# Kernel optimization log

Hardware: AMD Instinct MI355X
Metric: run time of the kernel (lower is better)

Reference implementation:

```python
import jax, jax.numpy as jnp
import numpy as np

SL, BS, HS = 2048, 2, 1024
FFN, E, TOP_K = 4096, 8, 2


def setup_inputs() -> dict:
    key = jax.random.key(0)
    k1, k2, k3, k4, k5 = jax.random.split(key, 5)
    x = jax.random.normal(k1, (SL, BS, HS), dtype=jnp.float32)
    expert_weights = jax.random.uniform(k2, (SL * BS, TOP_K), dtype=jnp.float32)
    expert_indices = jax.random.randint(k3, (SL * BS, TOP_K), 0, E, dtype=jnp.int32)
    w1 = jax.random.normal(k4, (E, HS, FFN), dtype=jnp.float32) * 0.02
    w2 = jax.random.normal(k5, (E, FFN, HS), dtype=jnp.float32) * 0.02
    return {"x": x, "expert_weights": expert_weights,
            "expert_indices": expert_indices, "w1": w1, "w2": w2}


def reference(x, expert_weights, expert_indices, w1, w2):
    # Dropless MoE: y[t] = sum_k expert_weights[t,k] * MLP_{expert_indices[t,k]}(x[t])
    # Equivalent to megablocks sort/gather/grouped-GEMM/scatter pipeline, expressed
    # as a fixed loop over the (small) expert axis with masked weighted combine.
    sl, bs, hs = x.shape
    xf = x.reshape(-1, hs)                       # [T, hs]
    ew = expert_weights.reshape(xf.shape[0], -1)  # [T, k]
    ei = expert_indices.reshape(xf.shape[0], -1)  # [T, k]
    out = jnp.zeros_like(xf)
    for e in range(w1.shape[0]):
        h = jnp.dot(jax.nn.gelu(jnp.dot(xf, w1[e])), w2[e])   # [T, hs]
        coef = jnp.sum(jnp.where(ei == e, ew, 0.0), axis=-1)  # [T]
        out = out + coef[:, None] * h
    return out.reshape(sl, bs, hs)
```

## Files before the change

### kernel.cpp

```cpp
#include <hip/hip_runtime.h>
#include <stdint.h>

#define SLEN 2048
#define BSZ  2
#define HSZ  1024
#define FFND 4096
#define NEXP 8
#define TOPK 2
#define NTOK (SLEN*BSZ)
#define NSLOT (NTOK*TOPK)

#define BM 128
#define BN 128
#define BK 32
#define STAGE (BM * BK)

#define KSPLIT 2
#define HALFK (FFND / KSPLIT)

using short8 = __attribute__((ext_vector_type(8))) short;
using f32x4  = __attribute__((ext_vector_type(4))) float;

typedef __attribute__((address_space(1))) const unsigned int gu32;
typedef __attribute__((address_space(3))) unsigned int lu32;

__device__ inline void async_copy16(const void* g, void* l){
  __builtin_amdgcn_global_load_lds((gu32*)g, (lu32*)l, 16, 0, 0);
}

__device__ inline unsigned short f2bf(float f){
  unsigned u = __builtin_bit_cast(unsigned, f);
  u += 0x7FFFu + ((u >> 16) & 1u);
  return (unsigned short)(u >> 16);
}

__device__ inline float gelu_tanh(float x){
  float u = 0.7978845608028654f * (x + 0.044715f * x * x * x);
  return 0.5f * x * (1.0f + tanhf(u));
}

__global__ __launch_bounds__(1024) void k_route(const int* __restrict__ ei,
                                                const float* __restrict__ ew,
                                                int* __restrict__ counts,
                                                int* __restrict__ offsets,
                                                int* __restrict__ rowT,
                                                float* __restrict__ rowC){
  __shared__ int hist[NEXP];
  __shared__ int fill[NEXP];
  const int tid = threadIdx.x;
  if (tid < NEXP) hist[tid] = 0;
  __syncthreads();
  int myE[NSLOT / 1024];
  #pragma unroll
  for (int p = 0; p < NSLOT / 1024; p++){
    myE[p] = ei[tid + p * 1024];
    atomicAdd(&hist[myE[p]], 1);
  }
  __syncthreads();
  if (tid == 0){
    int acc = 0;
    for (int e = 0; e < NEXP; e++){
      offsets[e] = acc; counts[e] = hist[e]; fill[e] = acc; acc += hist[e];
    }
  }
  __syncthreads();
  #pragma unroll
  for (int p = 0; p < NSLOT / 1024; p++){
    int i = tid + p * 1024;
    int slot = atomicAdd(&fill[myE[p]], 1);
    rowT[slot] = i >> 1;
    rowC[slot] = ew[i];
  }
}

__global__ void k_gather(const float* __restrict__ x, const int* __restrict__ rowT,
                         unsigned short* __restrict__ Xg){
  int slot = blockIdx.x;
  int t = rowT[slot];
  int c = threadIdx.x * 4;
  float4 v = *(const float4*)(x + (size_t)t * HSZ + c);
  ushort4 o;
  o.x = f2bf(v.x); o.y = f2bf(v.y); o.z = f2bf(v.z); o.w = f2bf(v.w);
  *(ushort4*)(Xg + (size_t)slot * HSZ + c) = o;
}

__global__ __launch_bounds__(256) void k_transpose2(const float* __restrict__ w1,
                                                    const float* __restrict__ w2,
                                                    unsigned short* __restrict__ Wt1,
                                                    unsigned short* __restrict__ Wt2){
  __shared__ unsigned short tile[64][65];
  const int tid = threadIdx.x;
  int z = blockIdx.y;
  const float* src; unsigned short* dst; int R, C, r0, c0;
  if (z < NEXP){
    src = w1 + (size_t)z * HSZ * FFND; dst = Wt1 + (size_t)z * HSZ * FFND;
    R = HSZ; C = FFND;
    c0 = (blockIdx.x & 63) * 64; r0 = (blockIdx.x >> 6) * 64;
  } else {
    z -= NEXP;
    src = w2 + (size_t)z * FFND * HSZ; dst = Wt2 + (size_t)z * FFND * HSZ;
    R = FFND; C = HSZ;
    c0 = (blockIdx.x & 15) * 64; r0 = (blockIdx.x >> 4) * 64;
  }
  #pragma unroll
  for (int p = 0; p < 4; p++){
    int r  = p * 16 + (tid >> 4);
    int cc = (tid & 15) * 4;
    float4 v = *(const float4*)(src + (size_t)(r0 + r) * C + c0 + cc);
    tile[r][cc]   = f2bf(v.x);
    tile[r][cc+1] = f2bf(v.y);
    tile[r][cc+2] = f2bf(v.z);
    tile[r][cc+3] = f2bf(v.w);
  }
  __syncthreads();
  #pragma unroll
  for (int p = 0; p < 4; p++){
    int c  = p * 16 + (tid >> 4);
    int rr = (tid & 15) * 4;
    ushort4 o;
    o.x = tile[rr][c]; o.y = tile[rr+1][c]; o.z = tile[rr+2][c]; o.w = tile[rr+3][c];
    *(ushort4*)(dst + (size_t)(c0 + c) * R + r0 + rr) = o;
  }
}

__device__ inline void gemm_core(const unsigned short* __restrict__ Ag, int lda, int rows,
                                 const unsigned short* __restrict__ Bg, int ldb, int K,
                                 unsigned short* As, unsigned short* Bs,
                                 f32x4 acc[4][4])
{
  const int tid  = threadIdx.x;
  const int lane = tid & 63;
  const int wid  = tid >> 6;
  const int wm   = (wid & 1) * 64;
  const int wn   = (wid >> 1) * 64;
  const int q    = lane >> 4;
  const int l16  = lane & 15;

  const int c0 = (wid * 2) * 64 + lane;
  const int c1 = c0 + 64;
  unsigned aoff0 = (unsigned)(min(c0 >> 2, rows - 1) * lda + (c0 & 3) * 8) * 2u;
  unsigned aoff1 = (unsigned)(min(c1 >> 2, rows - 1) * lda + (c1 & 3) * 8) * 2u;
  unsigned boff0 = (unsigned)((c0 >> 2) * ldb + (c0 & 3) * 8) * 2u;
  unsigned boff1 = (unsigned)((c1 >> 2) * ldb + (c1 & 3) * 8) * 2u;
  const char* A8 = (const char*)Ag;
  const char* B8 = (const char*)Bg;
  unsigned short* al0 = As + (wid * 2) * 512;
  unsigned short* bl0 = Bs + (wid * 2) * 512;

  auto stage = [&](int s){
    async_copy16(A8 + aoff0, al0 + s * STAGE);
    async_copy16(B8 + boff0, bl0 + s * STAGE);
    async_copy16(A8 + aoff1, al0 + s * STAGE + 512);
    async_copy16(B8 + boff1, bl0 + s * STAGE + 512);
    aoff0 += BK * 2; aoff1 += BK * 2; boff0 += BK * 2; boff1 += BK * 2;
  };

  const int niter = K / BK;
  stage(0);
  for (int k = 0; k < niter; k++){
    __syncthreads();
    if (k + 1 < niter) stage((k + 1) & 1);
    const unsigned short* Ak = As + (k & 1) * STAGE;
    const unsigned short* Bk = Bs + (k & 1) * STAGE;

    short8 af[4], bfr[4];
    #pragma unroll
    for (int i = 0; i < 4; i++)
      af[i] = *(const short8*)(Ak + (wm + i * 16 + l16) * BK + q * 8);
    #pragma unroll
    for (int j = 0; j < 4; j++)
      bfr[j] = *(const short8*)(Bk + (wn + j * 16 + l16) * BK + q * 8);

    #pragma unroll
    for (int i = 0; i < 4; i++)
      #pragma unroll
      for (int j = 0; j < 4; j++)
        acc[i][j] = __builtin_amdgcn_mfma_f32_16x16x32_bf16(af[i], bfr[j], acc[i][j], 0, 0, 0);
  }
}

__global__ __launch_bounds__(256) void k_gemm1(const unsigned short* __restrict__ Xg,
                                               const unsigned short* __restrict__ Wt1,
                                               unsigned short* __restrict__ H,
                                               const int* __restrict__ counts,
                                               const int* __restrict__ offsets)
{
  __shared__ unsigned short smem[4 * STAGE];
  unsigned short* As = smem;
  unsigned short* Bs = smem + 2 * STAGE;
  const int e    = blockIdx.z;
  const int cnt  = counts[e];
  const int mblk = blockIdx.y;
  if (mblk * BM >= cnt) return;
  const int n0   = blockIdx.x * BN;
  const int row0 = offsets[e] + mblk * BM;
  const int rows = min(BM, cnt - mblk * BM);

  f32x4 acc[4][4] = {};
  gemm_core(Xg + (size_t)row0 * HSZ, HSZ, rows,
            Wt1 + (size_t)e * HSZ * FFND + (size_t)n0 * HSZ, HSZ, HSZ, As, Bs, acc);
  __syncthreads();

  const int lane = threadIdx.x & 63, wid = threadIdx.x >> 6;
  const int wm = (wid & 1) * 64, wn = (wid >> 1) * 64;
  const int q = lane >> 4, l16 = lane & 15;

  unsigned short* scr = smem + wid * (16 * 68);
  #pragma unroll
  for (int i = 0; i < 4; i++){
    #pragma unroll
    for (int j = 0; j < 4; j++)
      #pragma unroll
      for (int r = 0; r < 4; r++)
        scr[(q * 4 + r) * 68 + j * 16 + l16] = f2bf(gelu_tanh(acc[i][j][r]));
    #pragma unroll
    for (int p = 0; p < 2; p++){
      int rr = p * 8 + (lane >> 3);
      int cc = (lane & 7) * 8;
      short8 v = *(const short8*)(scr + rr * 68 + cc);
      int grow = wm + i * 16 + rr;
      if (grow < rows)
        *(short8*)(H + (size_t)(row0 + grow) * FFND + n0 + wn + cc) = v;
    }
  }
}

__global__ __launch_bounds__(256, 4) void k_gemm2(const unsigned short* __restrict__ H,
                                                  const unsigned short* __restrict__ Wt2,
                                                  float* __restrict__ out,
                                                  const int* __restrict__ counts,
                                                  const int* __restrict__ offsets,
                                                  const int* __restrict__ rowT,
                                                  const float* __restrict__ rowC)
{
  __shared__ unsigned short smem[4 * STAGE];
  unsigned short* As = smem;
  unsigned short* Bs = smem + 2 * STAGE;
  const int e    = blockIdx.z;
  const int cnt  = counts[e];
  const int ks   = blockIdx.y % KSPLIT;
  const int mblk = blockIdx.y / KSPLIT;
  if (mblk * BM >= cnt) return;
  const int n0   = blockIdx.x * BN;
  const int row0 = offsets[e] + mblk * BM;
  const int rows = min(BM, cnt - mblk * BM);

  f32x4 acc[4][4] = {};
  gemm_core(H + (size_t)row0 * FFND + ks * HALFK, FFND, rows,
            Wt2 + (size_t)e * FFND * HSZ + (size_t)n0 * FFND + ks * HALFK, FFND,
            HALFK, As, Bs, acc);

  const int lane = threadIdx.x & 63, wid = threadIdx.x >> 6;
  const int wm = (wid & 1) * 64, wn = (wid >> 1) * 64;
  const int q = lane >> 4, l16 = lane & 15;
  #pragma unroll
  for (int i = 0; i < 4; i++)
    #pragma unroll
    for (int r = 0; r < 4; r++){
      int row = wm + i * 16 + q * 4 + r;
      if (row < rows){
        int g = row0 + row;
        float cf = rowC[g];
        float* op = out + (size_t)rowT[g] * HSZ + n0 + wn;
        #pragma unroll
        for (int j = 0; j < 4; j++)
          atomicAdd(op + j * 16 + l16, cf * acc[i][j][r]);
      }
    }
}

static inline size_t align_up(size_t v, size_t a){ return (v + a - 1) & ~(a - 1); }

extern "C" void kernel_launch(void* const* d_in, const int* in_sizes, int n_in,
                              void* d_out, int out_size, void* d_ws, size_t ws_size,
                              hipStream_t stream) {
  const float* x  = (const float*)d_in[0];
  const float* ew = (const float*)d_in[1];
  const int*   ei = (const int*)d_in[2];
  const float* w1 = (const float*)d_in[3];
  const float* w2 = (const float*)d_in[4];
  float* out = (float*)d_out;

  char* base = (char*)d_ws;
  size_t off = 0;
  int* counts  = (int*)(base + off); off += 64;
  int* offsets = (int*)(base + off); off = align_up(off + 64, 4096);
  int* rowT    = (int*)(base + off); off += (size_t)NSLOT * 4;
  float* rowC  = (float*)(base + off); off = align_up(off + (size_t)NSLOT * 4, 1 << 20);
  unsigned short* Xg  = (unsigned short*)(base + off); off = align_up(off + (size_t)NSLOT * HSZ * 2, 1 << 20);
  unsigned short* H   = (unsigned short*)(base + off); off = align_up(off + (size_t)NSLOT * FFND * 2, 1 << 20);
  unsigned short* Wt1 = (unsigned short*)(base + off); off = align_up(off + (size_t)NEXP * HSZ * FFND * 2, 1 << 20);
  unsigned short* Wt2 = (unsigned short*)(base + off); off += (size_t)NEXP * FFND * HSZ * 2;
  (void)ws_size;

  hipMemsetAsync(d_out, 0, (size_t)out_size * sizeof(float), stream);

  k_route <<<1, 1024, 0, stream>>>(ei, ew, counts, offsets, rowT, rowC);
  k_gather<<<NSLOT, 256, 0, stream>>>(x, rowT, Xg);

  k_transpose2<<<dim3(1024, 2 * NEXP), 256, 0, stream>>>(w1, w2, Wt1, Wt2);

  k_gemm1<<<dim3(FFND / BN, 64, NEXP), 256, 0, stream>>>(Xg, Wt1, H, counts, offsets);
  k_gemm2<<<dim3(HSZ / BN, 64 * KSPLIT, NEXP), 256, 0, stream>>>(H, Wt2, out, counts, offsets, rowT, rowC);
}
```

Baseline: 611.3 us.

## Use three-stage LDS ring with vmcnt-based waits in grouped GEMM core

Replaces the double-buffered LDS pipeline with a three-slot ring that keeps two async global-to-LDS stages in flight. Each iteration waits only for the oldest stage's loads via s_waitcnt vmcnt(4) plus a raw barrier, rather than a full __syncthreads. It also raises wave priority around the MFMA block and adds an occupancy hint of 4 to k_gemm1. This should hide more memory latency, at the cost of 50% more shared memory per block. On the final iterations it issues redundant loads without advancing the offsets.

```diff
diff --git a/kernel.cpp b/kernel.cpp
--- a/kernel.cpp
+++ b/kernel.cpp
@@ -14,6 +14,7 @@
 #define BN 128
 #define BK 32
 #define STAGE (BM * BK)
+#define RING 3
 
 #define KSPLIT 2
 #define HALFK (FFND / KSPLIT)
@@ -152,17 +153,24 @@
     async_copy16(B8 + boff0, bl0 + s * STAGE);
     async_copy16(A8 + aoff1, al0 + s * STAGE + 512);
     async_copy16(B8 + boff1, bl0 + s * STAGE + 512);
-    aoff0 += BK * 2; aoff1 += BK * 2; boff0 += BK * 2; boff1 += BK * 2;
   };
+  auto advance = [&](){ aoff0 += BK * 2; aoff1 += BK * 2; boff0 += BK * 2; boff1 += BK * 2; };
 
   const int niter = K / BK;
-  stage(0);
+  stage(0); advance();
+  stage(1); advance();
+
+  int rd = 0, wr2 = 2;
   for (int k = 0; k < niter; k++){
-    __syncthreads();
-    if (k + 1 < niter) stage((k + 1) & 1);
-    const unsigned short* Ak = As + (k & 1) * STAGE;
-    const unsigned short* Bk = Bs + (k & 1) * STAGE;
-
+    asm volatile("s_waitcnt vmcnt(4)" ::: "memory");
+    __builtin_amdgcn_s_barrier();
+    asm volatile("" ::: "memory");
+
+    stage(wr2);
+    if (k + 3 < niter) advance();
+
+    const unsigned short* Ak = As + rd * STAGE;
+    const unsigned short* Bk = Bs + rd * STAGE;
     short8 af[4], bfr[4];
     #pragma unroll
     for (int i = 0; i < 4; i++)
@@ -171,23 +179,31 @@
     for (int j = 0; j < 4; j++)
       bfr[j] = *(const short8*)(Bk + (wn + j * 16 + l16) * BK + q * 8);
 
+    __builtin_amdgcn_s_setprio(1);
     #pragma unroll
     for (int i = 0; i < 4; i++)
       #pragma unroll
       for (int j = 0; j < 4; j++)
         acc[i][j] = __builtin_amdgcn_mfma_f32_16x16x32_bf16(af[i], bfr[j], acc[i][j], 0, 0, 0);
-  }
-}
-
-__global__ __launch_bounds__(256) void k_gemm1(const unsigned short* __restrict__ Xg,
-                                               const unsigned short* __restrict__ Wt1,
-                                               unsigned short* __restrict__ H,
-                                               const int* __restrict__ counts,
-                                               const int* __restrict__ offsets)
+    __builtin_amdgcn_s_setprio(0);
+
+    rd  = (rd  + 1 == RING) ? 0 : rd  + 1;
+    wr2 = (wr2 + 1 == RING) ? 0 : wr2 + 1;
+  }
+  asm volatile("s_waitcnt vmcnt(0)" ::: "memory");
+  __builtin_amdgcn_s_barrier();
+  asm volatile("" ::: "memory");
+}
+
+__global__ __launch_bounds__(256, 4) void k_gemm1(const unsigned short* __restrict__ Xg,
+                                                  const unsigned short* __restrict__ Wt1,
+                                                  unsigned short* __restrict__ H,
+                                                  const int* __restrict__ counts,
+                                                  const int* __restrict__ offsets)
 {
-  __shared__ unsigned short smem[4 * STAGE];
+  __shared__ unsigned short smem[2 * RING * STAGE];
   unsigned short* As = smem;
-  unsigned short* Bs = smem + 2 * STAGE;
+  unsigned short* Bs = smem + RING * STAGE;
   const int e    = blockIdx.z;
   const int cnt  = counts[e];
   const int mblk = blockIdx.y;
@@ -233,9 +249,9 @@
                                                   const int* __restrict__ rowT,
                                                   const float* __restrict__ rowC)
 {
-  __shared__ unsigned short smem[4 * STAGE];
+  __shared__ unsigned short smem[2 * RING * STAGE];
   unsigned short* As = smem;
-  unsigned short* Bs = smem + 2 * STAGE;
+  unsigned short* Bs = smem + RING * STAGE;
   const int e    = blockIdx.z;
   const int cnt  = counts[e];
   const int ks   = blockIdx.y % KSPLIT;
```

Result: faster. 577.1 us (-5.6%).
